# Kernel optimization log

Hardware: AMD Instinct MI355X
Metric: run time of the kernel (lower is better)

Reference implementation:

```python
import jax, jax.numpy as jnp
import numpy as np

B, T = 2, 4096
TOK_DIM, POS_DIM = 64, 64
N_HEADS, HEAD_DIM = 8, 32
D_MODEL = 256


def setup_inputs() -> dict:
    key = jax.random.key(0)
    ks = jax.random.split(key, 5)
    s = 0.02
    return {
        "x": jax.random.normal(ks[0], (B, T, TOK_DIM + POS_DIM), dtype=jnp.float32),
        "Wq": jax.random.normal(ks[1], (POS_DIM, N_HEADS * HEAD_DIM), dtype=jnp.float32) * s,
        "Wk": jax.random.normal(ks[2], (POS_DIM, N_HEADS * HEAD_DIM), dtype=jnp.float32) * s,
        "Wv": jax.random.normal(ks[3], (TOK_DIM, N_HEADS * HEAD_DIM), dtype=jnp.float32) * s,
        "Wo": jax.random.normal(ks[4], (N_HEADS * HEAD_DIM, D_MODEL), dtype=jnp.float32) * s,
    }


def reference(x, Wq, Wk, Wv, Wo):
    Bb, Tt, _ = x.shape
    x_tok = x[:, :, :TOK_DIM]   # V comes from token dims
    x_pos = x[:, :, TOK_DIM:]   # Q,K come from positional dims

    # [B, T, H, Dh] -> [B, H, T, Dh]
    q = (x_pos @ Wq).reshape(Bb, Tt, N_HEADS, HEAD_DIM).transpose(0, 2, 1, 3)
    k = (x_pos @ Wk).reshape(Bb, Tt, N_HEADS, HEAD_DIM).transpose(0, 2, 1, 3)
    v = (x_tok @ Wv).reshape(Bb, Tt, N_HEADS, HEAD_DIM).transpose(0, 2, 1, 3)

    scale = 1.0 / jnp.sqrt(jnp.float32(HEAD_DIM))
    scores = jnp.einsum("bhqd,bhkd->bhqk", q, k) * scale  # [B,H,T,T]
    causal = jnp.tril(jnp.ones((Tt, Tt), dtype=bool))
    scores = jnp.where(causal[None, None, :, :], scores, -jnp.inf)
    attn = jax.nn.softmax(scores, axis=-1)

    out = jnp.einsum("bhqk,bhkd->bhqd", attn, v)          # [B,H,T,Dh]
    out = out.transpose(0, 2, 1, 3).reshape(Bb, Tt, N_HEADS * HEAD_DIM)
    return out @ Wo
```

## Files before the change

### kernel.cpp

```cpp
#include <hip/hip_runtime.h>

typedef __attribute__((ext_vector_type(8))) short bf16x8;
typedef __attribute__((ext_vector_type(4))) float f32x4;
typedef __attribute__((ext_vector_type(16))) float f32x16;

#define NB 2
#define SEQ 4096
#define NHD 8
#define HDIM 32
#define DMODEL 256

#define QSCALE 0.25503506f

__device__ __forceinline__ short f2bf(float f) {
  union { float f; unsigned u; } v; v.f = f;
  unsigned r = v.u + 0x7fffu + ((v.u >> 16) & 1u);
  return (short)(r >> 16);
}

__global__ __launch_bounds__(256) void proj_kernel(
    const float* __restrict__ x, const float* __restrict__ Wq,
    const float* __restrict__ Wk, const float* __restrict__ Wv,
    const float* __restrict__ Wo,
    short* __restrict__ Q, short* __restrict__ K, short* __restrict__ VT,
    short* __restrict__ WoT)
{
  __shared__ float xs[8][128];
  const int tid = threadIdx.x;
  const int row0 = blockIdx.x * 8;
  {
    const float4* src = (const float4*)(x + (size_t)row0 * 128);
    float4* dst = (float4*)xs;
    dst[tid] = src[tid];
  }
  if (blockIdx.x < 256)
    WoT[blockIdx.x * 256 + tid] = f2bf(Wo[tid * 256 + blockIdx.x]);
  __syncthreads();
  const int c = tid;
  float qa[8], ka[8], va[8];
#pragma unroll
  for (int r = 0; r < 8; ++r) { qa[r] = 0.f; ka[r] = 0.f; va[r] = 0.f; }
  for (int d4 = 0; d4 < 16; ++d4) {
    float wq[4], wk[4], wv[4];
#pragma unroll
    for (int j = 0; j < 4; ++j) {
      const int d = d4 * 4 + j;
      wq[j] = Wq[d * 256 + c];
      wk[j] = Wk[d * 256 + c];
      wv[j] = Wv[d * 256 + c];
    }
#pragma unroll
    for (int r = 0; r < 8; ++r) {
      const float4 xt = *(const float4*)&xs[r][d4 * 4];
      const float4 xp = *(const float4*)&xs[r][64 + d4 * 4];
      qa[r] += xp.x * wq[0] + xp.y * wq[1] + xp.z * wq[2] + xp.w * wq[3];
      ka[r] += xp.x * wk[0] + xp.y * wk[1] + xp.z * wk[2] + xp.w * wk[3];
      va[r] += xt.x * wv[0] + xt.y * wv[1] + xt.z * wv[2] + xt.w * wv[3];
    }
  }
  const int b = row0 >> 12;
  const int t0 = row0 & 4095;
  const int h = c >> 5, d = c & 31;
  const int bh = b * NHD + h;
#pragma unroll
  for (int r = 0; r < 8; ++r) {
    const int idx = (bh * SEQ + t0 + r) * HDIM + d;
    Q[idx] = f2bf(qa[r] * QSCALE);
    K[idx] = f2bf(ka[r]);
  }
  bf16x8 vv;
#pragma unroll
  for (int r = 0; r < 8; ++r) vv[r] = f2bf(va[r]);
  *(bf16x8*)&VT[(size_t)(bh * HDIM + d) * SEQ + t0] = vv;
}

__device__ __forceinline__ void score_to_p(const f32x16& S, bool masked, int hi, int l31,
                                           float& lsum, bf16x8& p0v, bf16x8& p1v)
{
  unsigned Wd[8];
  if (masked) {
#pragma unroll
    for (int i = 0; i < 8; ++i) {
      const int r0 = 2 * i;
      const int k0 = (r0 & 3) + ((r0 >> 2) << 3) + (hi << 2);
      float e0 = (k0     <= l31) ? __builtin_amdgcn_exp2f(S[r0])     : 0.f;
      float e1 = (k0 + 1 <= l31) ? __builtin_amdgcn_exp2f(S[r0 + 1]) : 0.f;
      lsum += e0 + e1;
      asm("v_cvt_pk_bf16_f32 %0, %1, %2" : "=v"(Wd[i]) : "v"(e0), "v"(e1));
    }
  } else {
#pragma unroll
    for (int i = 0; i < 8; ++i) {
      float e0 = __builtin_amdgcn_exp2f(S[2 * i]);
      float e1 = __builtin_amdgcn_exp2f(S[2 * i + 1]);
      lsum += e0 + e1;
      asm("v_cvt_pk_bf16_f32 %0, %1, %2" : "=v"(Wd[i]) : "v"(e0), "v"(e1));
    }
  }
  union { unsigned u[4]; bf16x8 v; } p0, p1;
  unsigned s;
  s = __shfl_xor((int)Wd[2], 32); p0.u[0] = hi ? s : Wd[0];
  s = __shfl_xor((int)Wd[0], 32); p0.u[2] = hi ? Wd[2] : s;
  s = __shfl_xor((int)Wd[3], 32); p0.u[1] = hi ? s : Wd[1];
  s = __shfl_xor((int)Wd[1], 32); p0.u[3] = hi ? Wd[3] : s;
  s = __shfl_xor((int)Wd[6], 32); p1.u[0] = hi ? s : Wd[4];
  s = __shfl_xor((int)Wd[4], 32); p1.u[2] = hi ? Wd[6] : s;
  s = __shfl_xor((int)Wd[7], 32); p1.u[1] = hi ? s : Wd[5];
  s = __shfl_xor((int)Wd[5], 32); p1.u[3] = hi ? Wd[7] : s;
  p0v = p0.v; p1v = p1.v;
}

__global__ __launch_bounds__(256, 4) void attn_kernel(
    const short* __restrict__ Q, const short* __restrict__ K,
    const short* __restrict__ VT, short* __restrict__ O)
{
  __shared__ float MG[8][17][64];

  const int flat = blockIdx.x;
  const int bh = (flat & 7) + (((flat >> 3) & 1) << 3);
  const int p = flat >> 4;
  const int tA = p, tB = 127 - p;
  const int q0A = tA << 5, q0B = tB << 5;
  const int ncA = tA + 1, ncB = tB + 1;

  const int w = threadIdx.x >> 6;
  const int lane = threadIdx.x & 63;
  const int l31 = lane & 31;
  const int hi = lane >> 5;

  const short* Kb  = K  + (size_t)bh * SEQ * HDIM;
  const short* VTb = VT + (size_t)bh * HDIM * SEQ;

  const short* qrowA = &Q[((size_t)bh * SEQ + q0A + l31) * HDIM + hi * 8];
  const bf16x8 qfA0 = *(const bf16x8*)qrowA;
  const bf16x8 qfA1 = *(const bf16x8*)(qrowA + 16);
  const short* qrowB = &Q[((size_t)bh * SEQ + q0B + l31) * HDIM + hi * 8];
  const bf16x8 qfB0 = *(const bf16x8*)qrowB;
  const bf16x8 qfB1 = *(const bf16x8*)(qrowB + 16);

  const f32x16 z16 = {0.f,0.f,0.f,0.f,0.f,0.f,0.f,0.f,0.f,0.f,0.f,0.f,0.f,0.f,0.f,0.f};
  f32x16 accA = z16, accB = z16;
  float lsumA = 0.f, lsumB = 0.f;

  int c = w;
  bf16x8 kf0, kf1, vf0, vf1;
  if (c < ncB) {
    const int kb = c << 5;
    const short* krow = &Kb[(size_t)(kb + l31) * HDIM + hi * 8];
    kf0 = *(const bf16x8*)krow;
    kf1 = *(const bf16x8*)(krow + 16);
    const short* vrow = &VTb[(size_t)l31 * SEQ + kb + hi * 8];
    vf0 = *(const bf16x8*)vrow;
    vf1 = *(const bf16x8*)(vrow + 16);
  }
  for (; c < ncB; c += 4) {
    const int kb = c << 5;
    const int cn = c + 4;
    bf16x8 kn0, kn1, vn0, vn1;
    if (cn < ncB) {
      const int kbn = cn << 5;
      const short* krow = &Kb[(size_t)(kbn + l31) * HDIM + hi * 8];
      kn0 = *(const bf16x8*)krow;
      kn1 = *(const bf16x8*)(krow + 16);
      const short* vrow = &VTb[(size_t)l31 * SEQ + kbn + hi * 8];
      vn0 = *(const bf16x8*)vrow;
      vn1 = *(const bf16x8*)(vrow + 16);
    }
    {
      f32x16 S = __builtin_amdgcn_mfma_f32_32x32x16_bf16(kf0, qfB0, z16, 0, 0, 0);
      S = __builtin_amdgcn_mfma_f32_32x32x16_bf16(kf1, qfB1, S, 0, 0, 0);
      bf16x8 p0v, p1v;
      score_to_p(S, kb == q0B, hi, l31, lsumB, p0v, p1v);
      accB = __builtin_amdgcn_mfma_f32_32x32x16_bf16(vf0, p0v, accB, 0, 0, 0);
      accB = __builtin_amdgcn_mfma_f32_32x32x16_bf16(vf1, p1v, accB, 0, 0, 0);
    }
    if (c < ncA) {
      f32x16 S = __builtin_amdgcn_mfma_f32_32x32x16_bf16(kf0, qfA0, z16, 0, 0, 0);
      S = __builtin_amdgcn_mfma_f32_32x32x16_bf16(kf1, qfA1, S, 0, 0, 0);
      bf16x8 p0v, p1v;
      score_to_p(S, kb == q0A, hi, l31, lsumA, p0v, p1v);
      accA = __builtin_amdgcn_mfma_f32_32x32x16_bf16(vf0, p0v, accA, 0, 0, 0);
      accA = __builtin_amdgcn_mfma_f32_32x32x16_bf16(vf1, p1v, accA, 0, 0, 0);
    }
    kf0 = kn0; kf1 = kn1; vf0 = vn0; vf1 = vn1;
  }

#pragma unroll
  for (int i = 0; i < 16; ++i) MG[w][i][lane] = accA[i];
  MG[w][16][lane] = lsumA;
#pragma unroll
  for (int i = 0; i < 16; ++i) MG[4 + w][i][lane] = accB[i];
  MG[4 + w][16][lane] = lsumB;
  __syncthreads();
  if (w < 2) {
    const int base = w << 2;
    const int q0 = w ? q0B : q0A;
    float fa[16];
#pragma unroll
    for (int i = 0; i < 16; ++i) fa[i] = 0.f;
    float fl = 0.f;
#pragma unroll
    for (int w2 = 0; w2 < 4; ++w2) {
#pragma unroll
      for (int i = 0; i < 16; ++i) fa[i] += MG[base + w2][i][lane];
      fl += MG[base + w2][16][lane] + MG[base + w2][16][lane ^ 32];
    }
    const float inv = 1.f / fl;
    const size_t obase = ((size_t)bh * SEQ + q0 + l31) * HDIM;
#pragma unroll
    for (int rg = 0; rg < 4; ++rg) {
      const int d0 = (rg << 3) + (hi << 2);
      short4 st;
      st.x = f2bf(fa[rg * 4 + 0] * inv);
      st.y = f2bf(fa[rg * 4 + 1] * inv);
      st.z = f2bf(fa[rg * 4 + 2] * inv);
      st.w = f2bf(fa[rg * 4 + 3] * inv);
      *(short4*)&O[obase + d0] = st;
    }
  }
}

__global__ __launch_bounds__(256) void ogemm_kernel(
    const short* __restrict__ O, const short* __restrict__ WoT, float* __restrict__ out)
{
  const int w = threadIdx.x >> 6;
  const int lane = threadIdx.x & 63;
  const int l15 = lane & 15, g = lane >> 4;
  const int m0 = blockIdx.x * 64 + w * 16;
  const int n0 = blockIdx.y * 64;
  const int b = m0 >> 12;
  const int t = (m0 & 4095) + l15;
  f32x4 acc[4];
#pragma unroll
  for (int i = 0; i < 4; ++i) acc[i] = (f32x4){0.f, 0.f, 0.f, 0.f};
#pragma unroll
  for (int ks = 0; ks < 8; ++ks) {
    const bf16x8 af = *(const bf16x8*)&O[(((size_t)b * NHD + ks) * SEQ + t) * HDIM + g * 8];
#pragma unroll
    for (int nt = 0; nt < 4; ++nt) {
      const bf16x8 bfr = *(const bf16x8*)&WoT[(n0 + nt * 16 + l15) * 256 + ks * 32 + g * 8];
      acc[nt] = __builtin_amdgcn_mfma_f32_16x16x32_bf16(af, bfr, acc[nt], 0, 0, 0);
    }
  }
#pragma unroll
  for (int nt = 0; nt < 4; ++nt)
#pragma unroll
    for (int r = 0; r < 4; ++r)
      out[(size_t)(m0 + (g << 2) + r) * 256 + n0 + nt * 16 + l15] = acc[nt][r];
}

extern "C" void kernel_launch(void* const* d_in, const int* in_sizes, int n_in,
                              void* d_out, int out_size, void* d_ws, size_t ws_size,
                              hipStream_t stream)
{
  const float* x  = (const float*)d_in[0];
  const float* Wq = (const float*)d_in[1];
  const float* Wk = (const float*)d_in[2];
  const float* Wv = (const float*)d_in[3];
  const float* Wo = (const float*)d_in[4];
  float* out = (float*)d_out;

  short* Q   = (short*)d_ws;
  short* K   = Q + 2097152;
  short* VT  = K + 2097152;
  short* O   = VT + 2097152;
  short* WoT = O + 2097152;

  proj_kernel<<<dim3(1024), dim3(256), 0, stream>>>(x, Wq, Wk, Wv, Wo, Q, K, VT, WoT);
  attn_kernel<<<dim3(1024), dim3(256), 0, stream>>>(Q, K, VT, O);
  ogemm_kernel<<<dim3(128, 4), dim3(256), 0, stream>>>(O, WoT, out);
}
```

Measured before the change: 136.8 us.

## Permute K rows to drop P shuffles, split attention loop, retile output GEMM

The projection now stores K rows in a permuted order inside each 32-row block. This lets the softmax output from the score MFMA feed the PV MFMA directly, without the eight cross-half lane shuffles. The attention loop is split into a phase that handles both query tiles and a phase that handles only the B tile, and the mask branch becomes a template specialisation, removing per-iteration conditionals. The output GEMM uses 32-column tiles with twice the blocks and software-prefetches the next A and B fragments, trading more redundant A loads for extra parallelism.

Measured after the change: 137.2 us. No clear change (+0.3%).

```diff
diff --git a/kernel.cpp b/kernel.cpp
--- a/kernel.cpp
+++ b/kernel.cpp
@@ -64,9 +64,10 @@
   const int bh = b * NHD + h;
 #pragma unroll
   for (int r = 0; r < 8; ++r) {
-    const int idx = (bh * SEQ + t0 + r) * HDIM + d;
-    Q[idx] = f2bf(qa[r] * QSCALE);
-    K[idx] = f2bf(ka[r]);
+    const int row = t0 + r;
+    Q[(bh * SEQ + row) * HDIM + d] = f2bf(qa[r] * QSCALE);
+    const int prow = (row & ~31) | (row & 19) | ((row & 4) << 1) | ((row & 8) >> 1);
+    K[(bh * SEQ + prow) * HDIM + d] = f2bf(ka[r]);
   }
   bf16x8 vv;
 #pragma unroll
@@ -74,39 +75,28 @@
   *(bf16x8*)&VT[(size_t)(bh * HDIM + d) * SEQ + t0] = vv;
 }
 
-__device__ __forceinline__ void score_to_p(const f32x16& S, bool masked, int hi, int l31,
+template <bool MASKED>
+__device__ __forceinline__ void score_to_p(const f32x16& S, int hi, int l31,
                                            float& lsum, bf16x8& p0v, bf16x8& p1v)
 {
-  unsigned Wd[8];
-  if (masked) {
-#pragma unroll
-    for (int i = 0; i < 8; ++i) {
-      const int r0 = 2 * i;
-      const int k0 = (r0 & 3) + ((r0 >> 2) << 3) + (hi << 2);
-      float e0 = (k0     <= l31) ? __builtin_amdgcn_exp2f(S[r0])     : 0.f;
-      float e1 = (k0 + 1 <= l31) ? __builtin_amdgcn_exp2f(S[r0 + 1]) : 0.f;
-      lsum += e0 + e1;
-      asm("v_cvt_pk_bf16_f32 %0, %1, %2" : "=v"(Wd[i]) : "v"(e0), "v"(e1));
-    }
-  } else {
-#pragma unroll
-    for (int i = 0; i < 8; ++i) {
-      float e0 = __builtin_amdgcn_exp2f(S[2 * i]);
-      float e1 = __builtin_amdgcn_exp2f(S[2 * i + 1]);
-      lsum += e0 + e1;
-      asm("v_cvt_pk_bf16_f32 %0, %1, %2" : "=v"(Wd[i]) : "v"(e0), "v"(e1));
-    }
-  }
   union { unsigned u[4]; bf16x8 v; } p0, p1;
-  unsigned s;
-  s = __shfl_xor((int)Wd[2], 32); p0.u[0] = hi ? s : Wd[0];
-  s = __shfl_xor((int)Wd[0], 32); p0.u[2] = hi ? Wd[2] : s;
-  s = __shfl_xor((int)Wd[3], 32); p0.u[1] = hi ? s : Wd[1];
-  s = __shfl_xor((int)Wd[1], 32); p0.u[3] = hi ? Wd[3] : s;
-  s = __shfl_xor((int)Wd[6], 32); p1.u[0] = hi ? s : Wd[4];
-  s = __shfl_xor((int)Wd[4], 32); p1.u[2] = hi ? Wd[6] : s;
-  s = __shfl_xor((int)Wd[7], 32); p1.u[1] = hi ? s : Wd[5];
-  s = __shfl_xor((int)Wd[5], 32); p1.u[3] = hi ? Wd[7] : s;
+#pragma unroll
+  for (int i = 0; i < 8; ++i) {
+    const int r0 = 2 * i;
+    float e0, e1;
+    if (MASKED) {
+      const int koff = (r0 & 3) + (((r0 >> 2) & 1) << 2) + (((r0 >> 3) & 1) << 4) + (hi << 3);
+      e0 = (koff     <= l31) ? __builtin_amdgcn_exp2f(S[r0])     : 0.f;
+      e1 = (koff + 1 <= l31) ? __builtin_amdgcn_exp2f(S[r0 + 1]) : 0.f;
+    } else {
+      e0 = __builtin_amdgcn_exp2f(S[r0]);
+      e1 = __builtin_amdgcn_exp2f(S[r0 + 1]);
+    }
+    lsum += e0 + e1;
+    unsigned wd;
+    asm("v_cvt_pk_bf16_f32 %0, %1, %2" : "=v"(wd) : "v"(e0), "v"(e1));
+    if (i < 4) p0.u[i] = wd; else p1.u[i - 4] = wd;
+  }
   p0v = p0.v; p1v = p1.v;
 }
 
@@ -144,7 +134,7 @@
 
   int c = w;
   bf16x8 kf0, kf1, vf0, vf1;
-  if (c < ncB) {
+  {
     const int kb = c << 5;
     const short* krow = &Kb[(size_t)(kb + l31) * HDIM + hi * 8];
     kf0 = *(const bf16x8*)krow;
@@ -153,6 +143,40 @@
     vf0 = *(const bf16x8*)vrow;
     vf1 = *(const bf16x8*)(vrow + 16);
   }
+
+  for (; c < ncA; c += 4) {
+    const int kb = c << 5;
+    const int cn = c + 4;
+    bf16x8 kn0, kn1, vn0, vn1;
+    if (cn < ncB) {
+      const int kbn = cn << 5;
+      const short* krow = &Kb[(size_t)(kbn + l31) * HDIM + hi * 8];
+      kn0 = *(const bf16x8*)krow;
+      kn1 = *(const bf16x8*)(krow + 16);
+      const short* vrow = &VTb[(size_t)l31 * SEQ + kbn + hi * 8];
+      vn0 = *(const bf16x8*)vrow;
+      vn1 = *(const bf16x8*)(vrow + 16);
+    }
+    {
+      f32x16 S = __builtin_amdgcn_mfma_f32_32x32x16_bf16(kf0, qfB0, z16, 0, 0, 0);
+      S = __builtin_amdgcn_mfma_f32_32x32x16_bf16(kf1, qfB1, S, 0, 0, 0);
+      bf16x8 p0v, p1v;
+      score_to_p<false>(S, hi, l31, lsumB, p0v, p1v);
+      accB = __builtin_amdgcn_mfma_f32_32x32x16_bf16(vf0, p0v, accB, 0, 0, 0);
+      accB = __builtin_amdgcn_mfma_f32_32x32x16_bf16(vf1, p1v, accB, 0, 0, 0);
+    }
+    {
+      f32x16 S = __builtin_amdgcn_mfma_f32_32x32x16_bf16(kf0, qfA0, z16, 0, 0, 0);
+      S = __builtin_amdgcn_mfma_f32_32x32x16_bf16(kf1, qfA1, S, 0, 0, 0);
+      bf16x8 p0v, p1v;
+      if (kb == q0A) score_to_p<true >(S, hi, l31, lsumA, p0v, p1v);
+      else           score_to_p<false>(S, hi, l31, lsumA, p0v, p1v);
+      accA = __builtin_amdgcn_mfma_f32_32x32x16_bf16(vf0, p0v, accA, 0, 0, 0);
+      accA = __builtin_amdgcn_mfma_f32_32x32x16_bf16(vf1, p1v, accA, 0, 0, 0);
+    }
+    kf0 = kn0; kf1 = kn1; vf0 = vn0; vf1 = vn1;
+  }
+
   for (; c < ncB; c += 4) {
     const int kb = c << 5;
     const int cn = c + 4;
@@ -166,22 +190,13 @@
       vn0 = *(const bf16x8*)vrow;
       vn1 = *(const bf16x8*)(vrow + 16);
     }
-    {
-      f32x16 S = __builtin_amdgcn_mfma_f32_32x32x16_bf16(kf0, qfB0, z16, 0, 0, 0);
-      S = __builtin_amdgcn_mfma_f32_32x32x16_bf16(kf1, qfB1, S, 0, 0, 0);
-      bf16x8 p0v, p1v;
-      score_to_p(S, kb == q0B, hi, l31, lsumB, p0v, p1v);
-      accB = __builtin_amdgcn_mfma_f32_32x32x16_bf16(vf0, p0v, accB, 0, 0, 0);
-      accB = __builtin_amdgcn_mfma_f32_32x32x16_bf16(vf1, p1v, accB, 0, 0, 0);
-    }
-    if (c < ncA) {
-      f32x16 S = __builtin_amdgcn_mfma_f32_32x32x16_bf16(kf0, qfA0, z16, 0, 0, 0);
-      S = __builtin_amdgcn_mfma_f32_32x32x16_bf16(kf1, qfA1, S, 0, 0, 0);
-      bf16x8 p0v, p1v;
-      score_to_p(S, kb == q0A, hi, l31, lsumA, p0v, p1v);
-      accA = __builtin_amdgcn_mfma_f32_32x32x16_bf16(vf0, p0v, accA, 0, 0, 0);
-      accA = __builtin_amdgcn_mfma_f32_32x32x16_bf16(vf1, p1v, accA, 0, 0, 0);
-    }
+    f32x16 S = __builtin_amdgcn_mfma_f32_32x32x16_bf16(kf0, qfB0, z16, 0, 0, 0);
+    S = __builtin_amdgcn_mfma_f32_32x32x16_bf16(kf1, qfB1, S, 0, 0, 0);
+    bf16x8 p0v, p1v;
+    if (kb == q0B) score_to_p<true >(S, hi, l31, lsumB, p0v, p1v);
+    else           score_to_p<false>(S, hi, l31, lsumB, p0v, p1v);
+    accB = __builtin_amdgcn_mfma_f32_32x32x16_bf16(vf0, p0v, accB, 0, 0, 0);
+    accB = __builtin_amdgcn_mfma_f32_32x32x16_bf16(vf1, p1v, accB, 0, 0, 0);
     kf0 = kn0; kf1 = kn1; vf0 = vn0; vf1 = vn1;
   }
 
@@ -227,26 +242,36 @@
   const int lane = threadIdx.x & 63;
   const int l15 = lane & 15, g = lane >> 4;
   const int m0 = blockIdx.x * 64 + w * 16;
-  const int n0 = blockIdx.y * 64;
+  const int n0 = blockIdx.y * 32;
   const int b = m0 >> 12;
   const int t = (m0 & 4095) + l15;
-  f32x4 acc[4];
-#pragma unroll
-  for (int i = 0; i < 4; ++i) acc[i] = (f32x4){0.f, 0.f, 0.f, 0.f};
+
+  const short* Ab = &O[(((size_t)b * NHD) * SEQ + t) * HDIM + g * 8];
+  const short* B0 = &WoT[(n0 + l15) * 256 + g * 8];
+  const short* B1 = &WoT[(n0 + 16 + l15) * 256 + g * 8];
+
+  f32x4 acc0 = {0.f, 0.f, 0.f, 0.f}, acc1 = {0.f, 0.f, 0.f, 0.f};
+  bf16x8 af = *(const bf16x8*)Ab;
+  bf16x8 b0 = *(const bf16x8*)B0;
+  bf16x8 b1 = *(const bf16x8*)B1;
 #pragma unroll
   for (int ks = 0; ks < 8; ++ks) {
-    const bf16x8 af = *(const bf16x8*)&O[(((size_t)b * NHD + ks) * SEQ + t) * HDIM + g * 8];
-#pragma unroll
-    for (int nt = 0; nt < 4; ++nt) {
-      const bf16x8 bfr = *(const bf16x8*)&WoT[(n0 + nt * 16 + l15) * 256 + ks * 32 + g * 8];
-      acc[nt] = __builtin_amdgcn_mfma_f32_16x16x32_bf16(af, bfr, acc[nt], 0, 0, 0);
-    }
-  }
-#pragma unroll
-  for (int nt = 0; nt < 4; ++nt)
-#pragma unroll
-    for (int r = 0; r < 4; ++r)
-      out[(size_t)(m0 + (g << 2) + r) * 256 + n0 + nt * 16 + l15] = acc[nt][r];
+    bf16x8 an, bn0, bn1;
+    if (ks < 7) {
+      an  = *(const bf16x8*)(Ab + (size_t)(ks + 1) * SEQ * HDIM);
+      bn0 = *(const bf16x8*)(B0 + (ks + 1) * 32);
+      bn1 = *(const bf16x8*)(B1 + (ks + 1) * 32);
+    }
+    acc0 = __builtin_amdgcn_mfma_f32_16x16x32_bf16(af, b0, acc0, 0, 0, 0);
+    acc1 = __builtin_amdgcn_mfma_f32_16x16x32_bf16(af, b1, acc1, 0, 0, 0);
+    af = an; b0 = bn0; b1 = bn1;
+  }
+#pragma unroll
+  for (int r = 0; r < 4; ++r) {
+    const size_t ro = (size_t)(m0 + (g << 2) + r) * 256 + n0 + l15;
+    out[ro] = acc0[r];
+    out[ro + 16] = acc1[r];
+  }
 }
 
 extern "C" void kernel_launch(void* const* d_in, const int* in_sizes, int n_in,
@@ -268,5 +293,5 @@
 
   proj_kernel<<<dim3(1024), dim3(256), 0, stream>>>(x, Wq, Wk, Wv, Wo, Q, K, VT, WoT);
   attn_kernel<<<dim3(1024), dim3(256), 0, stream>>>(Q, K, VT, O);
-  ogemm_kernel<<<dim3(128, 4), dim3(256), 0, stream>>>(O, WoT, out);
-}
+  ogemm_kernel<<<dim3(128, 8), dim3(256), 0, stream>>>(O, WoT, out);
+}
```
